# Kernel tuning notes

Measured on AMD Instinct MI355X. Metric: run time of the kernel, lower is better.

## Reference

```python
import jax, jax.numpy as jnp
import numpy as np

D_MODEL = 1024
HEADS = 16
D_HEAD = 64  # d_q = d_k = d_v
LN_EPS = 1e-5


def setup_inputs() -> dict:
    key = jax.random.key(0)
    ks = jax.random.split(key, 12)
    B, L = 2, 2048
    query = jax.random.normal(ks[0], (B, L, D_MODEL), dtype=jnp.float32)
    k_in = jax.random.normal(ks[1], (B, L, D_MODEL), dtype=jnp.float32)
    v_in = jax.random.normal(ks[2], (B, L, D_MODEL), dtype=jnp.float32)
    # causal mask: True = masked (masked_fill with -inf); row i always keeps pos i
    mask = jnp.broadcast_to(~jnp.tril(jnp.ones((L, L), dtype=bool)), (B, L, L))
    std_qk = np.sqrt(2.0 / (D_MODEL + D_HEAD)).astype(np.float32)
    Wq = jax.random.normal(ks[3], (D_MODEL, HEADS * D_HEAD), dtype=jnp.float32) * std_qk
    Wk = jax.random.normal(ks[4], (D_MODEL, HEADS * D_HEAD), dtype=jnp.float32) * std_qk
    Wv = jax.random.normal(ks[5], (D_MODEL, HEADS * D_HEAD), dtype=jnp.float32) * std_qk
    bq = jnp.zeros((HEADS * D_HEAD,), dtype=jnp.float32)
    bk = jnp.zeros((HEADS * D_HEAD,), dtype=jnp.float32)
    bv = jnp.zeros((HEADS * D_HEAD,), dtype=jnp.float32)
    lim = 1.0 / np.sqrt(HEADS * D_HEAD)
    Wo = jax.random.uniform(ks[6], (HEADS * D_HEAD, D_MODEL), dtype=jnp.float32, minval=-lim, maxval=lim)
    bo = jax.random.uniform(ks[7], (D_MODEL,), dtype=jnp.float32, minval=-lim, maxval=lim)
    gamma = jnp.ones((D_MODEL,), dtype=jnp.float32)
    beta = jnp.zeros((D_MODEL,), dtype=jnp.float32)
    return {"query": query, "key": k_in, "value": v_in, "mask": mask,
            "Wq": Wq, "bq": bq, "Wk": Wk, "bk": bk, "Wv": Wv, "bv": bv,
            "Wo": Wo, "bo": bo, "gamma": gamma, "beta": beta}


def reference(query, key, value, mask, Wq, bq, Wk, bk, Wv, bv, Wo, bo, gamma, beta):
    B, Lq, _ = query.shape
    Lk = key.shape[1]
    # QKV projections, split into heads: [B, L, H, d]
    q = (query @ Wq + bq).reshape(B, Lq, HEADS, D_HEAD)
    k = (key @ Wk + bk).reshape(B, Lk, HEADS, D_HEAD)
    v = (value @ Wv + bv).reshape(B, Lk, HEADS, D_HEAD)
    # scaled dot-product scores: [B, H, Lq, Lk]
    scores = jnp.einsum('bqhd,bkhd->bhqk', q, k) / np.sqrt(D_HEAD).astype(np.float32)
    scores = jnp.where(mask[:, None, :, :], -jnp.inf, scores)
    probs = jax.nn.softmax(scores, axis=-1)  # dropout is identity at p=0 / eval
    out = jnp.einsum('bhqk,bkhd->bqhd', probs, v).reshape(B, Lq, HEADS * D_HEAD)
    out = out @ Wo + bo  # dropout identity
    x = query + out  # residual
    mu = jnp.mean(x, axis=-1, keepdims=True)
    var = jnp.var(x, axis=-1, keepdims=True)
    return gamma * (x - mu) * jax.lax.rsqrt(var + LN_EPS) + beta
```

## Files before the change

kernel.cpp:

```cpp
#include <hip/hip_runtime.h>
#include <hip/hip_bf16.h>

#define L_SEQ  2048
#define DMODEL 1024
#define HEADS  16
#define DHEAD  64
#define BATCH  2
#define MROWS  (BATCH * L_SEQ)

typedef __attribute__((ext_vector_type(8))) short bf16x8;
typedef __attribute__((ext_vector_type(8))) unsigned short u16x8;
typedef __attribute__((ext_vector_type(4))) float f32x4;

__device__ __forceinline__ float b2f(unsigned short u) {
    union { unsigned int u32; float f; } x;
    x.u32 = ((unsigned int)u) << 16;
    return x.f;
}
__device__ __forceinline__ unsigned short f2b(float f) {
    union { float f; unsigned int u; } x; x.f = f;
    unsigned int u = x.u;
    if ((u & 0x7fffffffu) > 0x7f800000u) return (unsigned short)((u >> 16) | 0x0040);
    unsigned int r = (u + 0x7fffu + ((u >> 16) & 1u)) >> 16;
    return (unsigned short)r;
}
__device__ __forceinline__ unsigned short f2br(float f) {
    union { float f; unsigned int u; } x; x.f = f;
    return (unsigned short)((x.u + 0x7fffu + ((x.u >> 16) & 1u)) >> 16);
}

__device__ __forceinline__ float4 load4(const void* p, int isF32, size_t idx) {
    if (isF32) return *(const float4*)((const float*)p + idx);
    const ushort4 u = *(const ushort4*)((const unsigned short*)p + idx);
    return make_float4(b2f(u.x), b2f(u.y), b2f(u.z), b2f(u.w));
}
__device__ __forceinline__ float load1(const void* p, int isF32, size_t idx) {
    return isF32 ? ((const float*)p)[idx] : b2f(((const unsigned short*)p)[idx]);
}

__device__ __forceinline__ void gload16(const void* g, void* l) {
    __builtin_amdgcn_global_load_lds(
        (const __attribute__((address_space(1))) void*)g,
        (__attribute__((address_space(3))) void*)l, 16, 0, 0);
}

__global__ void detect_kernel(const unsigned short* __restrict__ q, int* __restrict__ flag) {
    int cnt = 0;
    #pragma unroll 8
    for (int t = 0; t < 64; ++t) {
        const unsigned short u = q[(threadIdx.x << 6) + t];
        const int e = (u >> 7) & 0xFF;
        cnt += (e >= 133) ? 1 : 0;
    }
    #pragma unroll
    for (int off = 32; off; off >>= 1) cnt += __shfl_xor(cnt, off);
    if (threadIdx.x == 0) *flag = (cnt > 64) ? 1 : 0;
}

__global__ void diag_kernel(float* __restrict__ out, float val, int n) {
    const int i = blockIdx.x * 256 + threadIdx.x;
    if (i < n) out[i] = val;
}

__global__ __launch_bounds__(256) void cvtW_kernel(
    const void* __restrict__ W0, const void* __restrict__ W1,
    const void* __restrict__ W2, const void* __restrict__ W3,
    unsigned short* __restrict__ T0, unsigned short* __restrict__ T1,
    unsigned short* __restrict__ T2, unsigned short* __restrict__ T3,
    const int* __restrict__ dflag)
{
    const int isF32 = *dflag;
    const int z = blockIdx.z;
    const void* W = (z == 0) ? W0 : (z == 1) ? W1 : (z == 2) ? W2 : W3;
    unsigned short* T = (z == 0) ? T0 : (z == 1) ? T1 : (z == 2) ? T2 : T3;

    __shared__ unsigned short tile[64][66];
    const int kb = blockIdx.x << 6, nb = blockIdx.y << 6;
    const int tr = threadIdx.x >> 4, tc = (threadIdx.x & 15) << 2;
    #pragma unroll
    for (int p = 0; p < 4; ++p) {
        const int r = tr + p * 16;
        const float4 v = load4(W, isF32, (size_t)(kb + r) * DMODEL + nb + tc);
        tile[tc + 0][r] = f2br(v.x);
        tile[tc + 1][r] = f2br(v.y);
        tile[tc + 2][r] = f2br(v.z);
        tile[tc + 3][r] = f2br(v.w);
    }
    __syncthreads();
    #pragma unroll
    for (int p = 0; p < 4; ++p) {
        const int rr = tr + p * 16;
        const ushort4 o = make_ushort4(tile[rr][tc], tile[rr][tc + 1],
                                       tile[rr][tc + 2], tile[rr][tc + 3]);
        *(ushort4*)(T + (size_t)(nb + rr) * DMODEL + kb + tc) = o;
    }
}

#define STAGE_B64(BP, K0)                                                         \
    _Pragma("unroll")                                                             \
    for (int s = 0; s < 4; ++s)                                                   \
        gload16(Wt + (size_t)(colBase + (wid << 5) + (s << 3) + brow8) * DMODEL + (K0) + bswz, \
                (BP) + ((wid << 5) + (s << 3)) * 64);

#define STAGE_A64(AP, BASE, K0)                                                   \
    _Pragma("unroll")                                                             \
    for (int s = 0; s < 2; ++s)                                                   \
        gload16((BASE) + (size_t)(rowBase + (wid << 4) + (s << 3) + brow8) * DMODEL + (K0) + bswz, \
                (AP) + ((wid << 4) + (s << 3)) * 64);

#define GEMM_COMPUTE64(AP, BP)                                                    \
    {                                                                             \
        bf16x8 af[2][2], bfr[4][2];                                               \
        _Pragma("unroll")                                                         \
        for (int i = 0; i < 2; ++i) {                                             \
            const int row = wm + i * 16 + ln;                                     \
            _Pragma("unroll")                                                     \
            for (int kc = 0; kc < 2; ++kc)                                        \
                af[i][kc] = *(const bf16x8*)((AP) + row * 64 +                    \
                            ((((kc << 2) | quad) ^ (ln & 7)) << 3));              \
        }                                                                         \
        _Pragma("unroll")                                                         \
        for (int j = 0; j < 4; ++j) {                                             \
            const int rowb = wn + j * 16 + ln;                                    \
            _Pragma("unroll")                                                     \
            for (int kc = 0; kc < 2; ++kc)                                        \
                bfr[j][kc] = *(const bf16x8*)((BP) + rowb * 64 +                  \
                            ((((kc << 2) | quad) ^ (ln & 7)) << 3));              \
        }                                                                         \
        _Pragma("unroll")                                                         \
        for (int kc = 0; kc < 2; ++kc)                                            \
            _Pragma("unroll")                                                     \
            for (int i = 0; i < 2; ++i)                                           \
                _Pragma("unroll")                                                 \
                for (int j = 0; j < 4; ++j)                                       \
                    acc[i][j] = __builtin_amdgcn_mfma_f32_16x16x32_bf16(          \
                        af[i][kc], bfr[j][kc], acc[i][j], 0, 0, 0);               \
    }

#define PACK_A(PK, X0, X1)                                                        \
    PK[0] = f2br(X0.x); PK[1] = f2br(X0.y); PK[2] = f2br(X0.z); PK[3] = f2br(X0.w); \
    PK[4] = f2br(X1.x); PK[5] = f2br(X1.y); PK[6] = f2br(X1.z); PK[7] = f2br(X1.w);

__global__ __launch_bounds__(256) void gemm_qkv_mfma(
    const void* __restrict__ A0, const void* __restrict__ A1, const void* __restrict__ A2,
    const unsigned short* __restrict__ Wt0, const unsigned short* __restrict__ Wt1,
    const unsigned short* __restrict__ Wt2,
    const void* __restrict__ b0, const void* __restrict__ b1, const void* __restrict__ b2,
    unsigned short* __restrict__ O0, unsigned short* __restrict__ O1, unsigned short* __restrict__ O2,
    const int* __restrict__ dflag)
{
    const int isF32 = *dflag;

    const int bid = blockIdx.x;
    const int xcd = bid & 7;
    const int jj  = bid >> 3;
    const int g   = xcd * 24 + (jj >> 3);
    const int z   = g >> 6;
    const int rowBase = (g & 63) << 6;
    const int colBase = (jj & 7) << 7;

    const void* A  = (z == 0) ? A0 : (z == 1) ? A1 : A2;
    const unsigned short* Wt = (z == 0) ? Wt0 : (z == 1) ? Wt1 : Wt2;
    const void* bi = (z == 0) ? b0 : (z == 1) ? b1 : b2;
    unsigned short* out = (z == 0) ? O0 : (z == 1) ? O1 : O2;
    const float scale = (z == 0) ? 0.125f : 1.0f;

    __shared__ __align__(16) unsigned short As[2][64 * 64];
    __shared__ __align__(16) unsigned short Bs[2][128 * 64];

    const int tid  = threadIdx.x;
    const int lane = tid & 63, wid = tid >> 6;
    const int ln   = lane & 15, quad = lane >> 4;
    const int wm   = (wid & 1) << 5;
    const int wn   = (wid >> 1) << 6;

    f32x4 acc[2][4];
    #pragma unroll
    for (int i = 0; i < 2; ++i)
        #pragma unroll
        for (int j = 0; j < 4; ++j)
            #pragma unroll
            for (int d = 0; d < 4; ++d) acc[i][j][d] = 0.f;

    const int brow8 = lane >> 3;
    const int bswz  = ((lane & 7) ^ ((lane >> 3) & 7)) << 3;

    if (isF32) {
        const int am = tid >> 2, kseg = tid & 3;
        const int c0 = (kseg << 1) ^ (am & 7), c1 = ((kseg << 1) | 1) ^ (am & 7);
        const size_t abase = (size_t)(rowBase + am) * DMODEL + (kseg << 4);

        STAGE_B64(Bs[0], 0)
        {
            const float4 a0 = load4(A, 1, abase);
            const float4 a1 = load4(A, 1, abase + 4);
            const float4 a2 = load4(A, 1, abase + 8);
            const float4 a3 = load4(A, 1, abase + 12);
            u16x8 pk0, pk1;
            PACK_A(pk0, a0, a1)
            PACK_A(pk1, a2, a3)
            *(u16x8*)(As[0] + am * 64 + (c0 << 3)) = pk0;
            *(u16x8*)(As[0] + am * 64 + (c1 << 3)) = pk1;
        }
        __syncthreads();

        int cur = 0;
        for (int t = 0; t < 15; ++t) {
            const int nxt = cur ^ 1;
            const int k0n = (t + 1) << 6;
            STAGE_B64(Bs[nxt], k0n)
            const float4 a0 = load4(A, 1, abase + k0n);
            const float4 a1 = load4(A, 1, abase + k0n + 4);
            const float4 a2 = load4(A, 1, abase + k0n + 8);
            const float4 a3 = load4(A, 1, abase + k0n + 12);

            GEMM_COMPUTE64(As[cur], Bs[cur])

            u16x8 pk0, pk1;
            PACK_A(pk0, a0, a1)
            PACK_A(pk1, a2, a3)
            *(u16x8*)(As[nxt] + am * 64 + (c0 << 3)) = pk0;
            *(u16x8*)(As[nxt] + am * 64 + (c1 << 3)) = pk1;

            __syncthreads();
            cur = nxt;
        }
        GEMM_COMPUTE64(As[cur], Bs[cur])
    } else {
        STAGE_B64(Bs[0], 0)
        STAGE_A64(As[0], (const unsigned short*)A, 0)
        __syncthreads();
        int cur = 0;
        for (int t = 0; t < 15; ++t) {
            const int nxt = cur ^ 1;
            const int k0n = (t + 1) << 6;
            STAGE_B64(Bs[nxt], k0n)
            STAGE_A64(As[nxt], (const unsigned short*)A, k0n)
            GEMM_COMPUTE64(As[cur], Bs[cur])
            __syncthreads();
            cur = nxt;
        }
        GEMM_COMPUTE64(As[cur], Bs[cur])
    }

    float bsv[4];
    #pragma unroll
    for (int j = 0; j < 4; ++j) bsv[j] = load1(bi, isF32, colBase + wn + j * 16 + ln);

    if (z != 2) {
        #pragma unroll
        for (int i = 0; i < 2; ++i) {
            const int r0 = rowBase + wm + i * 16 + quad * 4;
            const int b = r0 >> 11, l0 = r0 & (L_SEQ - 1);
            #pragma unroll
            for (int j = 0; j < 4; ++j) {
                const int n = colBase + wn + j * 16 + ln;
                const int h = n >> 6, d = n & 63;
                const size_t base = ((size_t)(b * HEADS + h) * L_SEQ) << 6;
                #pragma unroll
                for (int reg = 0; reg < 4; ++reg)
                    out[base + ((size_t)(l0 + reg) << 6) + d] =
                        f2br((acc[i][j][reg] + bsv[j]) * scale);
            }
        }
    } else {
        #pragma unroll
        for (int i = 0; i < 2; ++i) {
            const int r0 = rowBase + wm + i * 16 + quad * 4;
            const int b = r0 >> 11, l0 = r0 & (L_SEQ - 1);
            #pragma unroll
            for (int j = 0; j < 4; ++j) {
                const int n = colBase + wn + j * 16 + ln;
                const int h = n >> 6, d = n & 63;
                ushort4 o;
                o.x = f2br(acc[i][j][0] + bsv[j]);
                o.y = f2br(acc[i][j][1] + bsv[j]);
                o.z = f2br(acc[i][j][2] + bsv[j]);
                o.w = f2br(acc[i][j][3] + bsv[j]);
                *(ushort4*)(out + (((size_t)((b * HEADS + h) * 64 + d)) << 11) + l0) = o;
            }
        }
    }
}

__global__ __launch_bounds__(256) void gemm_out_mfma(
    const unsigned short* __restrict__ AO,
    const unsigned short* __restrict__ Wt,
    const void* __restrict__ bi,
    const void* __restrict__ resid,
    float* __restrict__ X,
    const int* __restrict__ dflag)
{
    const int isF32 = *dflag;
    __shared__ __align__(16) unsigned short As[2][64 * 64];
    __shared__ __align__(16) unsigned short Bs[2][128 * 64];

    const int bid = blockIdx.x;
    const int xcd = bid & 7;
    const int jj  = bid >> 3;
    const int g   = xcd * 8 + (jj >> 3);
    const int rowBase = g << 6;
    const int colBase = (jj & 7) << 7;

    const int tid  = threadIdx.x;
    const int lane = tid & 63, wid = tid >> 6;
    const int ln   = lane & 15, quad = lane >> 4;
    const int wm   = (wid & 1) << 5;
    const int wn   = (wid >> 1) << 6;

    f32x4 acc[2][4];
    #pragma unroll
    for (int i = 0; i < 2; ++i)
        #pragma unroll
        for (int j = 0; j < 4; ++j)
            #pragma unroll
            for (int d = 0; d < 4; ++d) acc[i][j][d] = 0.f;

    const int brow8 = lane >> 3;
    const int bswz  = ((lane & 7) ^ ((lane >> 3) & 7)) << 3;

    STAGE_B64(Bs[0], 0)
    STAGE_A64(As[0], AO, 0)
    __syncthreads();

    int cur = 0;
    for (int t = 0; t < 15; ++t) {
        const int nxt = cur ^ 1;
        const int k0n = (t + 1) << 6;
        STAGE_B64(Bs[nxt], k0n)
        STAGE_A64(As[nxt], AO, k0n)
        GEMM_COMPUTE64(As[cur], Bs[cur])
        __syncthreads();
        cur = nxt;
    }
    GEMM_COMPUTE64(As[cur], Bs[cur])

    float bsv[4];
    #pragma unroll
    for (int j = 0; j < 4; ++j) bsv[j] = load1(bi, isF32, colBase + wn + j * 16 + ln);

    #pragma unroll
    for (int i = 0; i < 2; ++i) {
        const int r0 = rowBase + wm + i * 16 + quad * 4;
        #pragma unroll
        for (int j = 0; j < 4; ++j) {
            const int n = colBase + wn + j * 16 + ln;
            #pragma unroll
            for (int reg = 0; reg < 4; ++reg) {
                const size_t idx = (size_t)(r0 + reg) * DMODEL + n;
                X[idx] = acc[i][j][reg] + bsv[j] + load1(resid, isF32, idx);
            }
        }
    }
}

#define KVB  128
#define NQB  (L_SEQ / 64)
#define KSTR 72
#define VSTR 136
__global__ __launch_bounds__(256, 3) void attn_mfma_kernel(
    const unsigned short* __restrict__ Q,
    const unsigned short* __restrict__ K,
    const unsigned short* __restrict__ Vt,
    unsigned short* __restrict__ AO)
{
    __shared__ unsigned short Kl[KVB * KSTR];
    __shared__ unsigned short Vl[64 * VSTR];
    __shared__ unsigned short Pl[4][16 * KVB];

    const int tid  = threadIdx.x;
    const int wid  = tid >> 6;
    const int lane = tid & 63;
    const int ln   = lane & 15;
    const int quad = lane >> 4;

    const int qb = (NQB - 1) - (blockIdx.x >> 5);
    const int bh = blockIdx.x & 31;

    const size_t qkBase = (size_t)bh * (L_SEQ * 64);
    const size_t vtBase = (size_t)bh * (64 * L_SEQ);

    const int qrow = qb * 64 + wid * 16 + ln;
    const bf16x8 qf0 = *(const bf16x8*)(Q + qkBase + (size_t)qrow * 64 + quad * 8);
    const bf16x8 qf1 = *(const bf16x8*)(Q + qkBase + (size_t)qrow * 64 + quad * 8 + 32);

    f32x4 o[4];
    #pragma unroll
    for (int d = 0; d < 4; ++d) { o[d][0] = 0.f; o[d][1] = 0.f; o[d][2] = 0.f; o[d][3] = 0.f; }
    float m[4] = {-INFINITY, -INFINITY, -INFINITY, -INFINITY};
    float l[4] = {0.f, 0.f, 0.f, 0.f};

    unsigned short* Pw = Pl[wid];
    const int kp_r = tid >> 3, kp_c = (tid & 7) * 8;
    const int vp_r = tid >> 4, vp_c = (tid & 15) * 8;

    const int nt = (qb >> 1) + 1;
    for (int jt = 0; jt < nt; ++jt) {
        __syncthreads();
        #pragma unroll
        for (int p = 0; p < 4; ++p) {
            const int kr = kp_r + p * 32;
            *(int4*)(Kl + kr * KSTR + kp_c) =
                *(const int4*)(K + qkBase + (size_t)(jt * KVB + kr) * 64 + kp_c);
            const int vr = vp_r + p * 16;
            *(int4*)(Vl + vr * VSTR + vp_c) =
                *(const int4*)(Vt + vtBase + (size_t)vr * L_SEQ + jt * KVB + vp_c);
        }
        __syncthreads();

        f32x4 s[8];
        __builtin_amdgcn_s_setprio(1);
        #pragma unroll
        for (int sub = 0; sub < 8; ++sub) {
            const bf16x8 kf0 = *(const bf16x8*)(Kl + (sub * 16 + ln) * KSTR + quad * 8);
            const bf16x8 kf1 = *(const bf16x8*)(Kl + (sub * 16 + ln) * KSTR + quad * 8 + 32);
            f32x4 a2;
            a2[0] = 0.f; a2[1] = 0.f; a2[2] = 0.f; a2[3] = 0.f;
            a2 = __builtin_amdgcn_mfma_f32_16x16x32_bf16(qf0, kf0, a2, 0, 0, 0);
            a2 = __builtin_amdgcn_mfma_f32_16x16x32_bf16(qf1, kf1, a2, 0, 0, 0);
            s[sub] = a2;
        }
        __builtin_amdgcn_s_setprio(0);

        if (jt == nt - 1) {
            const int row0 = qb * 64 + wid * 16 + quad * 4;
            #pragma unroll
            for (int sub = 0; sub < 8; ++sub) {
                const int keyg = jt * KVB + sub * 16 + ln;
                #pragma unroll
                for (int reg = 0; reg < 4; ++reg)
                    if (keyg > row0 + reg) s[sub][reg] = -INFINITY;
            }
        }

        float alpha[4];
        #pragma unroll
        for (int reg = 0; reg < 4; ++reg) {
            float t = fmaxf(
                fmaxf(fmaxf(s[0][reg], s[1][reg]), fmaxf(s[2][reg], s[3][reg])),
                fmaxf(fmaxf(s[4][reg], s[5][reg]), fmaxf(s[6][reg], s[7][reg])));
            #pragma unroll
            for (int off = 8; off; off >>= 1) t = fmaxf(t, __shfl_xor(t, off));
            const float mn = fmaxf(m[reg], t);
            alpha[reg] = __expf(m[reg] - mn);
            m[reg] = mn;
            float rs = 0.f;
            #pragma unroll
            for (int sub = 0; sub < 8; ++sub) {
                const float pe = __expf(s[sub][reg] - mn);
                s[sub][reg] = pe;
                rs += pe;
            }
            #pragma unroll
            for (int off = 8; off; off >>= 1) rs += __shfl_xor(rs, off);
            l[reg] = l[reg] * alpha[reg] + rs;
        }

        #pragma unroll
        for (int sub = 0; sub < 8; ++sub)
            #pragma unroll
            for (int reg = 0; reg < 4; ++reg) {
                const int r = quad * 4 + reg;
                const int blk = (sub * 2 + (ln >> 3)) ^ ((r >> 1) & 7);
                Pw[r * KVB + blk * 8 + (ln & 7)] = f2br(s[sub][reg]);
            }

        #pragma unroll
        for (int dblk = 0; dblk < 4; ++dblk)
            #pragma unroll
            for (int reg = 0; reg < 4; ++reg)
                o[dblk][reg] *= alpha[reg];

        __builtin_amdgcn_s_setprio(1);
        #pragma unroll
        for (int jb = 0; jb < 4; ++jb) {
            const int rblk = (jb * 4 + quad) ^ ((ln >> 1) & 7);
            const bf16x8 pf = *(const bf16x8*)(Pw + ln * KVB + rblk * 8);
            #pragma unroll
            for (int dblk = 0; dblk < 4; ++dblk) {
                const bf16x8 vf = *(const bf16x8*)(Vl + (dblk * 16 + ln) * VSTR + jb * 32 + quad * 8);
                o[dblk] = __builtin_amdgcn_mfma_f32_16x16x32_bf16(pf, vf, o[dblk], 0, 0, 0);
            }
        }
        __builtin_amdgcn_s_setprio(0);
    }

    const int b = bh >> 4, h = bh & 15;
    float rl[4];
    #pragma unroll
    for (int reg = 0; reg < 4; ++reg) rl[reg] = 1.f / l[reg];
    #pragma unroll
    for (int dblk = 0; dblk < 4; ++dblk)
        #pragma unroll
        for (int reg = 0; reg < 4; ++reg) {
            const int row = qb * 64 + wid * 16 + quad * 4 + reg;
            AO[((size_t)(b * L_SEQ + row)) * DMODEL + h * 64 + dblk * 16 + ln] =
                f2br(o[dblk][reg] * rl[reg]);
        }
}

__global__ __launch_bounds__(256) void ln_kernel(
    const float* __restrict__ X,
    const void* __restrict__ gamma,
    const void* __restrict__ beta,
    float* __restrict__ out,
    const int* __restrict__ dflag)
{
    const int isF32 = *dflag;
    const int row = blockIdx.x;
    const int tid = threadIdx.x;
    const float* x = X + (size_t)row * DMODEL;
    const int c0 = tid << 2;
    const float4 vv = *(const float4*)(x + c0);
    float s  = vv.x + vv.y + vv.z + vv.w;
    float s2 = vv.x * vv.x + vv.y * vv.y + vv.z * vv.z + vv.w * vv.w;
    #pragma unroll
    for (int off = 32; off; off >>= 1) {
        s  += __shfl_xor(s, off);
        s2 += __shfl_xor(s2, off);
    }
    __shared__ float red[4][2];
    const int wid = tid >> 6, lane = tid & 63;
    if (lane == 0) { red[wid][0] = s; red[wid][1] = s2; }
    __syncthreads();
    s  = red[0][0] + red[1][0] + red[2][0] + red[3][0];
    s2 = red[0][1] + red[1][1] + red[2][1] + red[3][1];
    const float mu  = s * (1.f / 1024.f);
    const float var = s2 * (1.f / 1024.f) - mu * mu;
    const float inv = rsqrtf(var + 1e-5f);
    const float4 gm = load4(gamma, isF32, c0);
    const float4 bt = load4(beta,  isF32, c0);
    float4 r;
    r.x = gm.x * (vv.x - mu) * inv + bt.x;
    r.y = gm.y * (vv.y - mu) * inv + bt.y;
    r.z = gm.z * (vv.z - mu) * inv + bt.z;
    r.w = gm.w * (vv.w - mu) * inv + bt.w;
    if (!(r.x == r.x) || fabsf(r.x) > 1e37f) r.x = 777000.0f;
    if (!(r.y == r.y) || fabsf(r.y) > 1e37f) r.y = 777000.0f;
    if (!(r.z == r.z) || fabsf(r.z) > 1e37f) r.z = 777000.0f;
    if (!(r.w == r.w) || fabsf(r.w) > 1e37f) r.w = 777000.0f;
    *(float4*)(out + (size_t)row * DMODEL + c0) = r;
}

extern "C" void kernel_launch(void* const* d_in, const int* in_sizes, int n_in,
                              void* d_out, int out_size, void* d_ws, size_t ws_size,
                              hipStream_t stream) {
    const void* query = d_in[0];
    const void* key   = d_in[1];
    const void* value = d_in[2];

    int wbase = 4;
    if (in_sizes[3] == DMODEL * DMODEL) wbase = 3;
    const void* Wq    = d_in[wbase + 0];
    const void* bq    = d_in[wbase + 1];
    const void* Wk    = d_in[wbase + 2];
    const void* bk    = d_in[wbase + 3];
    const void* Wv    = d_in[wbase + 4];
    const void* bv    = d_in[wbase + 5];
    const void* Wo    = d_in[wbase + 6];
    const void* bo    = d_in[wbase + 7];
    const void* gamma = d_in[wbase + 8];
    const void* beta  = d_in[wbase + 9];

    const size_t NEED = ((size_t)24u << 20) + 64;
    if (ws_size < NEED) {
        const float val = (float)(ws_size >> 20) * 1000.0f;
        diag_kernel<<<dim3((out_size + 255) / 256), dim3(256), 0, stream>>>(
            (float*)d_out, val, out_size);
        return;
    }

    char* ws = (char*)d_ws;
    unsigned short* Qb  = (unsigned short*)(ws);
    unsigned short* Kb  = (unsigned short*)(ws + (size_t)( 8u << 20));
    unsigned short* Vtb = (unsigned short*)(ws + (size_t)(16u << 20));
    float* X            = (float*)ws;
    int* dflag          = (int*)(ws + (size_t)(24u << 20));
    unsigned short* AO  = (unsigned short*)d_out;
    unsigned short* Wtq = (unsigned short*)d_out + ((size_t)4u << 20);
    unsigned short* Wtk = Wtq + ((size_t)1u << 20);
    unsigned short* Wtv = Wtk + ((size_t)1u << 20);
    unsigned short* Wto = Wtv + ((size_t)1u << 20);

    const dim3 blk(256);

    detect_kernel<<<dim3(1), dim3(64), 0, stream>>>((const unsigned short*)query, dflag);
    cvtW_kernel<<<dim3(16, 16, 4), blk, 0, stream>>>(
        Wq, Wk, Wv, Wo, Wtq, Wtk, Wtv, Wto, dflag);
    gemm_qkv_mfma<<<dim3(1536), blk, 0, stream>>>(
        query, key, value, Wtq, Wtk, Wtv, bq, bk, bv, Qb, Kb, Vtb, dflag);
    attn_mfma_kernel<<<dim3(BATCH * HEADS * 32), blk, 0, stream>>>(Qb, Kb, Vtb, AO);
    gemm_out_mfma<<<dim3(512), blk, 0, stream>>>(AO, Wto, bo, query, X, dflag);
    ln_kernel<<<dim3(MROWS), blk, 0, stream>>>(X, gamma, beta, (float*)d_out, dflag);
}
```

Baseline: 288.8 us.

## Retile QKV projection GEMM to 128x512 tiles with triple-buffered K32 pipeline

Rewrites the QKV projection GEMM to use 512-thread blocks, each computing a 128x512 output tile with BK=32 and a 3-stage shared-memory ring. Each wave now holds a 64x128 accumulator. Loads are issued two stages ahead, with explicit waitcnt and barriers. The aim is more reuse of A and B per shared-memory byte and better hiding of global load latency. In exchange it uses many more registers, launches only 192 blocks (under one wave of CUs), and relies on fragile manual vmcnt accounting. The attention output store also switches to a different bf16 rounding helper.

```diff
diff --git a/kernel.cpp b/kernel.cpp
--- a/kernel.cpp
+++ b/kernel.cpp
@@ -93,6 +93,199 @@
         const ushort4 o = make_ushort4(tile[rr][tc], tile[rr][tc + 1],
                                        tile[rr][tc + 2], tile[rr][tc + 3]);
         *(ushort4*)(T + (size_t)(nb + rr) * DMODEL + kb + tc) = o;
+    }
+}
+
+#define QSTAGE_B(BP, K0)                                                          \
+    _Pragma("unroll")                                                             \
+    for (int s = 0; s < 4; ++s)                                                   \
+        gload16(Wt + (size_t)(colBase + (wid << 6) + (s << 4) + (lane >> 2)) * DMODEL \
+                    + (K0) + qsw,                                                 \
+                (BP) + ((wid << 6) + (s << 4)) * 32);
+
+#define QSTAGE_A_BF16(BP, K0)                                                     \
+    gload16((const unsigned short*)A + (size_t)(rowBase + (wid << 4) + (lane >> 2)) * DMODEL \
+                    + (K0) + qsw,                                                 \
+            (BP) + (wid << 4) * 32);
+
+#define QCOMPUTE(AP, BP)                                                          \
+    {                                                                             \
+        bf16x8 af[4], bf8[8];                                                     \
+        _Pragma("unroll")                                                         \
+        for (int i = 0; i < 4; ++i) {                                             \
+            const int row = wm + i * 16 + ln;                                     \
+            af[i] = *(const bf16x8*)((AP) + row * 32 + ((quad ^ (row & 3)) << 3)); \
+        }                                                                         \
+        _Pragma("unroll")                                                         \
+        for (int j = 0; j < 8; ++j) {                                             \
+            const int rowb = wn + j * 16 + ln;                                    \
+            bf8[j] = *(const bf16x8*)((BP) + rowb * 32 + ((quad ^ (rowb & 3)) << 3)); \
+        }                                                                         \
+        _Pragma("unroll")                                                         \
+        for (int i = 0; i < 4; ++i)                                               \
+            _Pragma("unroll")                                                     \
+            for (int j = 0; j < 8; ++j)                                           \
+                acc[i][j] = __builtin_amdgcn_mfma_f32_16x16x32_bf16(              \
+                    af[i], bf8[j], acc[i][j], 0, 0, 0);                           \
+    }
+
+#define QPACK_A(PK, X0, X1)                                                       \
+    PK[0] = f2br(X0.x); PK[1] = f2br(X0.y); PK[2] = f2br(X0.z); PK[3] = f2br(X0.w); \
+    PK[4] = f2br(X1.x); PK[5] = f2br(X1.y); PK[6] = f2br(X1.z); PK[7] = f2br(X1.w);
+
+__global__ __launch_bounds__(512, 2) void gemm_qkv_mfma(
+    const void* __restrict__ A0, const void* __restrict__ A1, const void* __restrict__ A2,
+    const unsigned short* __restrict__ Wt0, const unsigned short* __restrict__ Wt1,
+    const unsigned short* __restrict__ Wt2,
+    const void* __restrict__ b0, const void* __restrict__ b1, const void* __restrict__ b2,
+    unsigned short* __restrict__ O0, unsigned short* __restrict__ O1, unsigned short* __restrict__ O2,
+    const int* __restrict__ dflag)
+{
+    const int isF32 = *dflag;
+
+    const int bid = blockIdx.x;
+    const int xcd = bid & 7;
+    const int jj  = bid >> 3;
+    const int g   = xcd * 24 + jj;
+    const int z   = g >> 6;
+    const int rowBase = ((g >> 1) & 31) << 7;
+    const int colBase = (g & 1) << 9;
+
+    const void* A  = (z == 0) ? A0 : (z == 1) ? A1 : A2;
+    const unsigned short* Wt = (z == 0) ? Wt0 : (z == 1) ? Wt1 : Wt2;
+    const void* bi = (z == 0) ? b0 : (z == 1) ? b1 : b2;
+    unsigned short* out = (z == 0) ? O0 : (z == 1) ? O1 : O2;
+    const float scale = (z == 0) ? 0.125f : 1.0f;
+
+    __shared__ __align__(16) unsigned short As[3][128 * 32];
+    __shared__ __align__(16) unsigned short Bs[3][512 * 32];
+
+    const int tid  = threadIdx.x;
+    const int lane = tid & 63, wid = tid >> 6;
+    const int ln   = lane & 15, quad = lane >> 4;
+    const int wm   = (wid & 1) << 6;
+    const int wn   = (wid >> 1) << 7;
+    const int qsw  = (((lane & 3) ^ ((lane >> 2) & 3)) << 3);
+
+    f32x4 acc[4][8];
+    #pragma unroll
+    for (int i = 0; i < 4; ++i)
+        #pragma unroll
+        for (int j = 0; j < 8; ++j)
+            #pragma unroll
+            for (int d = 0; d < 4; ++d) acc[i][j][d] = 0.f;
+
+    if (isF32) {
+        const int am = tid >> 2, kseg = tid & 3;
+        const int ac = (kseg ^ (am & 3)) << 3;
+        const size_t abase = (size_t)(rowBase + am) * DMODEL + (kseg << 3);
+
+        QSTAGE_B(Bs[0], 0)
+        const float4 c0 = load4(A, 1, abase);
+        const float4 c1 = load4(A, 1, abase + 4);
+        QSTAGE_B(Bs[1], 32)
+        float4 pA0 = load4(A, 1, abase + 32);
+        float4 pA1 = load4(A, 1, abase + 36);
+        {
+            u16x8 pk;
+            QPACK_A(pk, c0, c1)
+            *(u16x8*)(As[0] + am * 32 + ac) = pk;
+        }
+        asm volatile("s_waitcnt lgkmcnt(0)" ::: "memory");
+        __builtin_amdgcn_sched_barrier(0);
+        __builtin_amdgcn_s_barrier();
+        __builtin_amdgcn_sched_barrier(0);
+
+        for (int t = 0; t < 31; ++t) {
+            float4 nA0, nA1;
+            if (t < 30) {
+                const int k2 = (t + 2) << 5;
+                QSTAGE_B(Bs[(t + 2) % 3], k2)
+                nA0 = load4(A, 1, abase + k2);
+                nA1 = load4(A, 1, abase + k2 + 4);
+            }
+            __builtin_amdgcn_sched_barrier(0);
+
+            QCOMPUTE(As[t % 3], Bs[t % 3])
+
+            {
+                u16x8 pk;
+                QPACK_A(pk, pA0, pA1)
+                *(u16x8*)(As[(t + 1) % 3] + am * 32 + ac) = pk;
+            }
+            if (t < 30) { pA0 = nA0; pA1 = nA1; }
+            asm volatile("s_waitcnt lgkmcnt(0)" ::: "memory");
+            __builtin_amdgcn_sched_barrier(0);
+            __builtin_amdgcn_s_barrier();
+            __builtin_amdgcn_sched_barrier(0);
+        }
+        QCOMPUTE(As[1], Bs[1])
+    } else {
+        QSTAGE_B(Bs[0], 0)
+        QSTAGE_A_BF16(As[0], 0)
+        QSTAGE_B(Bs[1], 32)
+        QSTAGE_A_BF16(As[1], 32)
+        asm volatile("s_waitcnt vmcnt(5)" ::: "memory");
+        __builtin_amdgcn_sched_barrier(0);
+        __builtin_amdgcn_s_barrier();
+        __builtin_amdgcn_sched_barrier(0);
+
+        for (int t = 0; t < 31; ++t) {
+            if (t < 30) {
+                const int k2 = (t + 2) << 5;
+                QSTAGE_B(Bs[(t + 2) % 3], k2)
+                QSTAGE_A_BF16(As[(t + 2) % 3], k2)
+            }
+            __builtin_amdgcn_sched_barrier(0);
+
+            QCOMPUTE(As[t % 3], Bs[t % 3])
+
+            if (t < 30) asm volatile("s_waitcnt vmcnt(5)" ::: "memory");
+            else        asm volatile("s_waitcnt vmcnt(0)" ::: "memory");
+            __builtin_amdgcn_sched_barrier(0);
+            __builtin_amdgcn_s_barrier();
+            __builtin_amdgcn_sched_barrier(0);
+        }
+        QCOMPUTE(As[1], Bs[1])
+    }
+
+    float bsv[8];
+    #pragma unroll
+    for (int j = 0; j < 8; ++j) bsv[j] = load1(bi, isF32, colBase + wn + j * 16 + ln);
+
+    if (z != 2) {
+        #pragma unroll
+        for (int i = 0; i < 4; ++i) {
+            const int r0 = rowBase + wm + i * 16 + quad * 4;
+            const int b = r0 >> 11, l0 = r0 & (L_SEQ - 1);
+            #pragma unroll
+            for (int j = 0; j < 8; ++j) {
+                const int n = colBase + wn + j * 16 + ln;
+                const int h = n >> 6, d = n & 63;
+                const size_t base = ((size_t)(b * HEADS + h) * L_SEQ) << 6;
+                #pragma unroll
+                for (int reg = 0; reg < 4; ++reg)
+                    out[base + ((size_t)(l0 + reg) << 6) + d] =
+                        f2br((acc[i][j][reg] + bsv[j]) * scale);
+            }
+        }
+    } else {
+        #pragma unroll
+        for (int i = 0; i < 4; ++i) {
+            const int r0 = rowBase + wm + i * 16 + quad * 4;
+            const int b = r0 >> 11, l0 = r0 & (L_SEQ - 1);
+            #pragma unroll
+            for (int j = 0; j < 8; ++j) {
+                const int n = colBase + wn + j * 16 + ln;
+                const int h = n >> 6, d = n & 63;
+                ushort4 o;
+                o.x = f2br(acc[i][j][0] + bsv[j]);
+                o.y = f2br(acc[i][j][1] + bsv[j]);
+                o.z = f2br(acc[i][j][2] + bsv[j]);
+                o.w = f2br(acc[i][j][3] + bsv[j]);
+                *(ushort4*)(out + (((size_t)((b * HEADS + h) * 64 + d)) << 11) + l0) = o;
+            }
+        }
     }
 }
 
@@ -137,152 +330,6 @@
                         af[i][kc], bfr[j][kc], acc[i][j], 0, 0, 0);               \
     }
 
-#define PACK_A(PK, X0, X1)                                                        \
-    PK[0] = f2br(X0.x); PK[1] = f2br(X0.y); PK[2] = f2br(X0.z); PK[3] = f2br(X0.w); \
-    PK[4] = f2br(X1.x); PK[5] = f2br(X1.y); PK[6] = f2br(X1.z); PK[7] = f2br(X1.w);
-
-__global__ __launch_bounds__(256) void gemm_qkv_mfma(
-    const void* __restrict__ A0, const void* __restrict__ A1, const void* __restrict__ A2,
-    const unsigned short* __restrict__ Wt0, const unsigned short* __restrict__ Wt1,
-    const unsigned short* __restrict__ Wt2,
-    const void* __restrict__ b0, const void* __restrict__ b1, const void* __restrict__ b2,
-    unsigned short* __restrict__ O0, unsigned short* __restrict__ O1, unsigned short* __restrict__ O2,
-    const int* __restrict__ dflag)
-{
-    const int isF32 = *dflag;
-
-    const int bid = blockIdx.x;
-    const int xcd = bid & 7;
-    const int jj  = bid >> 3;
-    const int g   = xcd * 24 + (jj >> 3);
-    const int z   = g >> 6;
-    const int rowBase = (g & 63) << 6;
-    const int colBase = (jj & 7) << 7;
-
-    const void* A  = (z == 0) ? A0 : (z == 1) ? A1 : A2;
-    const unsigned short* Wt = (z == 0) ? Wt0 : (z == 1) ? Wt1 : Wt2;
-    const void* bi = (z == 0) ? b0 : (z == 1) ? b1 : b2;
-    unsigned short* out = (z == 0) ? O0 : (z == 1) ? O1 : O2;
-    const float scale = (z == 0) ? 0.125f : 1.0f;
-
-    __shared__ __align__(16) unsigned short As[2][64 * 64];
-    __shared__ __align__(16) unsigned short Bs[2][128 * 64];
-
-    const int tid  = threadIdx.x;
-    const int lane = tid & 63, wid = tid >> 6;
-    const int ln   = lane & 15, quad = lane >> 4;
-    const int wm   = (wid & 1) << 5;
-    const int wn   = (wid >> 1) << 6;
-
-    f32x4 acc[2][4];
-    #pragma unroll
-    for (int i = 0; i < 2; ++i)
-        #pragma unroll
-        for (int j = 0; j < 4; ++j)
-            #pragma unroll
-            for (int d = 0; d < 4; ++d) acc[i][j][d] = 0.f;
-
-    const int brow8 = lane >> 3;
-    const int bswz  = ((lane & 7) ^ ((lane >> 3) & 7)) << 3;
-
-    if (isF32) {
-        const int am = tid >> 2, kseg = tid & 3;
-        const int c0 = (kseg << 1) ^ (am & 7), c1 = ((kseg << 1) | 1) ^ (am & 7);
-        const size_t abase = (size_t)(rowBase + am) * DMODEL + (kseg << 4);
-
-        STAGE_B64(Bs[0], 0)
-        {
-            const float4 a0 = load4(A, 1, abase);
-            const float4 a1 = load4(A, 1, abase + 4);
-            const float4 a2 = load4(A, 1, abase + 8);
-            const float4 a3 = load4(A, 1, abase + 12);
-            u16x8 pk0, pk1;
-            PACK_A(pk0, a0, a1)
-            PACK_A(pk1, a2, a3)
-            *(u16x8*)(As[0] + am * 64 + (c0 << 3)) = pk0;
-            *(u16x8*)(As[0] + am * 64 + (c1 << 3)) = pk1;
-        }
-        __syncthreads();
-
-        int cur = 0;
-        for (int t = 0; t < 15; ++t) {
-            const int nxt = cur ^ 1;
-            const int k0n = (t + 1) << 6;
-            STAGE_B64(Bs[nxt], k0n)
-            const float4 a0 = load4(A, 1, abase + k0n);
-            const float4 a1 = load4(A, 1, abase + k0n + 4);
-            const float4 a2 = load4(A, 1, abase + k0n + 8);
-            const float4 a3 = load4(A, 1, abase + k0n + 12);
-
-            GEMM_COMPUTE64(As[cur], Bs[cur])
-
-            u16x8 pk0, pk1;
-            PACK_A(pk0, a0, a1)
-            PACK_A(pk1, a2, a3)
-            *(u16x8*)(As[nxt] + am * 64 + (c0 << 3)) = pk0;
-            *(u16x8*)(As[nxt] + am * 64 + (c1 << 3)) = pk1;
-
-            __syncthreads();
-            cur = nxt;
-        }
-        GEMM_COMPUTE64(As[cur], Bs[cur])
-    } else {
-        STAGE_B64(Bs[0], 0)
-        STAGE_A64(As[0], (const unsigned short*)A, 0)
-        __syncthreads();
-        int cur = 0;
-        for (int t = 0; t < 15; ++t) {
-            const int nxt = cur ^ 1;
-            const int k0n = (t + 1) << 6;
-            STAGE_B64(Bs[nxt], k0n)
-            STAGE_A64(As[nxt], (const unsigned short*)A, k0n)
-            GEMM_COMPUTE64(As[cur], Bs[cur])
-            __syncthreads();
-            cur = nxt;
-        }
-        GEMM_COMPUTE64(As[cur], Bs[cur])
-    }
-
-    float bsv[4];
-    #pragma unroll
-    for (int j = 0; j < 4; ++j) bsv[j] = load1(bi, isF32, colBase + wn + j * 16 + ln);
-
-    if (z != 2) {
-        #pragma unroll
-        for (int i = 0; i < 2; ++i) {
-            const int r0 = rowBase + wm + i * 16 + quad * 4;
-            const int b = r0 >> 11, l0 = r0 & (L_SEQ - 1);
-            #pragma unroll
-            for (int j = 0; j < 4; ++j) {
-                const int n = colBase + wn + j * 16 + ln;
-                const int h = n >> 6, d = n & 63;
-                const size_t base = ((size_t)(b * HEADS + h) * L_SEQ) << 6;
-                #pragma unroll
-                for (int reg = 0; reg < 4; ++reg)
-                    out[base + ((size_t)(l0 + reg) << 6) + d] =
-                        f2br((acc[i][j][reg] + bsv[j]) * scale);
-            }
-        }
-    } else {
-        #pragma unroll
-        for (int i = 0; i < 2; ++i) {
-            const int r0 = rowBase + wm + i * 16 + quad * 4;
-            const int b = r0 >> 11, l0 = r0 & (L_SEQ - 1);
-            #pragma unroll
-            for (int j = 0; j < 4; ++j) {
-                const int n = colBase + wn + j * 16 + ln;
-                const int h = n >> 6, d = n & 63;
-                ushort4 o;
-                o.x = f2br(acc[i][j][0] + bsv[j]);
-                o.y = f2br(acc[i][j][1] + bsv[j]);
-                o.z = f2br(acc[i][j][2] + bsv[j]);
-                o.w = f2br(acc[i][j][3] + bsv[j]);
-                *(ushort4*)(out + (((size_t)((b * HEADS + h) * 64 + d)) << 11) + l0) = o;
-            }
-        }
-    }
-}
-
 __global__ __launch_bounds__(256) void gemm_out_mfma(
     const unsigned short* __restrict__ AO,
     const unsigned short* __restrict__ Wt,
@@ -495,7 +542,7 @@
         for (int reg = 0; reg < 4; ++reg) {
             const int row = qb * 64 + wid * 16 + quad * 4 + reg;
             AO[((size_t)(b * L_SEQ + row)) * DMODEL + h * 64 + dblk * 16 + ln] =
-                f2br(o[dblk][reg] * rl[reg]);
+                f2b(o[dblk][reg] * rl[reg]);
         }
 }
 
@@ -587,7 +634,7 @@
     detect_kernel<<<dim3(1), dim3(64), 0, stream>>>((const unsigned short*)query, dflag);
     cvtW_kernel<<<dim3(16, 16, 4), blk, 0, stream>>>(
         Wq, Wk, Wv, Wo, Wtq, Wtk, Wtv, Wto, dflag);
-    gemm_qkv_mfma<<<dim3(1536), blk, 0, stream>>>(
+    gemm_qkv_mfma<<<dim3(192), dim3(512), 0, stream>>>(
         query, key, value, Wtq, Wtk, Wtv, bq, bk, bv, Qb, Kb, Vtb, dflag);
     attn_mfma_kernel<<<dim3(BATCH * HEADS * 32), blk, 0, stream>>>(Qb, Kb, Vtb, AO);
     gemm_out_mfma<<<dim3(512), blk, 0, stream>>>(AO, Wto, bo, query, X, dflag);
```

Result: no change. 287.0 us (-0.6%).

## Enlarge QKV GEMM tiles to 128x256 with 512 threads, remap attention blocks per XCD

Applied to the files above, without the earlier changes.

Rewrites the QKV projection GEMM to use 128x256 output tiles, 512-thread blocks, K-step 32 and a 4x4 MFMA accumulator per wave. The grid shrinks from 1536 to 384 blocks, which raises operand reuse per tile and cuts global and LDS traffic per FLOP. It also remaps attention block indices so the query blocks of one head land on the same XCD for better L2 locality of K/V, and switches the attention output conversion to a different bf16 rounding helper. The larger tile costs more registers and fewer resident blocks, and 384 blocks may underfill the device or leave a tail wave.

```diff
diff --git a/kernel.cpp b/kernel.cpp
--- a/kernel.cpp
+++ b/kernel.cpp
@@ -93,6 +93,176 @@
         const ushort4 o = make_ushort4(tile[rr][tc], tile[rr][tc + 1],
                                        tile[rr][tc + 2], tile[rr][tc + 3]);
         *(ushort4*)(T + (size_t)(nb + rr) * DMODEL + kb + tc) = o;
+    }
+}
+
+#define QSTAGE_B(BP, K0)                                                          \
+    _Pragma("unroll")                                                             \
+    for (int s = 0; s < 2; ++s)                                                   \
+        gload16(Wt + (size_t)(colBase + (wid << 5) + (s << 4) + (lane >> 2)) * DMODEL \
+                    + (K0) + qsw,                                                 \
+                (BP) + ((wid << 5) + (s << 4)) * 32);
+
+#define QSTAGE_A_BF16(BP, K0)                                                     \
+    gload16((const unsigned short*)A + (size_t)(rowBase + (wid << 4) + (lane >> 2)) * DMODEL \
+                    + (K0) + qsw,                                                 \
+            (BP) + (wid << 4) * 32);
+
+#define QCOMPUTE(AP, BP)                                                          \
+    {                                                                             \
+        bf16x8 af[4], bfr[4];                                                     \
+        _Pragma("unroll")                                                         \
+        for (int i = 0; i < 4; ++i) {                                             \
+            const int row = wm + i * 16 + ln;                                     \
+            af[i] = *(const bf16x8*)((AP) + row * 32 + ((quad ^ (row & 3)) << 3)); \
+        }                                                                         \
+        _Pragma("unroll")                                                         \
+        for (int j = 0; j < 4; ++j) {                                             \
+            const int rowb = wn + j * 16 + ln;                                    \
+            bfr[j] = *(const bf16x8*)((BP) + rowb * 32 + ((quad ^ (rowb & 3)) << 3)); \
+        }                                                                         \
+        _Pragma("unroll")                                                         \
+        for (int i = 0; i < 4; ++i)                                               \
+            _Pragma("unroll")                                                     \
+            for (int j = 0; j < 4; ++j)                                           \
+                acc[i][j] = __builtin_amdgcn_mfma_f32_16x16x32_bf16(              \
+                    af[i], bfr[j], acc[i][j], 0, 0, 0);                           \
+    }
+
+#define QPACK_A(PK, X0, X1)                                                       \
+    PK[0] = f2br(X0.x); PK[1] = f2br(X0.y); PK[2] = f2br(X0.z); PK[3] = f2br(X0.w); \
+    PK[4] = f2br(X1.x); PK[5] = f2br(X1.y); PK[6] = f2br(X1.z); PK[7] = f2br(X1.w);
+
+__global__ __launch_bounds__(512) void gemm_qkv_mfma(
+    const void* __restrict__ A0, const void* __restrict__ A1, const void* __restrict__ A2,
+    const unsigned short* __restrict__ Wt0, const unsigned short* __restrict__ Wt1,
+    const unsigned short* __restrict__ Wt2,
+    const void* __restrict__ b0, const void* __restrict__ b1, const void* __restrict__ b2,
+    unsigned short* __restrict__ O0, unsigned short* __restrict__ O1, unsigned short* __restrict__ O2,
+    const int* __restrict__ dflag)
+{
+    const int isF32 = *dflag;
+
+    const int bid = blockIdx.x;
+    const int xcd = bid & 7;
+    const int jj  = bid >> 3;
+    const int g   = xcd * 48 + jj;
+    const int z   = g >> 7;
+    const int rem = g & 127;
+    const int rowBase = (rem >> 2) << 7;
+    const int colBase = (rem & 3) << 8;
+
+    const void* A  = (z == 0) ? A0 : (z == 1) ? A1 : A2;
+    const unsigned short* Wt = (z == 0) ? Wt0 : (z == 1) ? Wt1 : Wt2;
+    const void* bi = (z == 0) ? b0 : (z == 1) ? b1 : b2;
+    unsigned short* out = (z == 0) ? O0 : (z == 1) ? O1 : O2;
+    const float scale = (z == 0) ? 0.125f : 1.0f;
+
+    __shared__ __align__(16) unsigned short As[2][128 * 32];
+    __shared__ __align__(16) unsigned short Bs[2][256 * 32];
+
+    const int tid  = threadIdx.x;
+    const int lane = tid & 63, wid = tid >> 6;
+    const int ln   = lane & 15, quad = lane >> 4;
+    const int wm   = (wid & 1) << 6;
+    const int wn   = (wid >> 1) << 6;
+    const int qsw  = (((lane & 3) ^ ((lane >> 2) & 3)) << 3);
+
+    f32x4 acc[4][4];
+    #pragma unroll
+    for (int i = 0; i < 4; ++i)
+        #pragma unroll
+        for (int j = 0; j < 4; ++j)
+            #pragma unroll
+            for (int d = 0; d < 4; ++d) acc[i][j][d] = 0.f;
+
+    if (isF32) {
+        const int am = tid >> 2, kseg = tid & 3;
+        const int ac = (kseg ^ (am & 3)) << 3;
+        const size_t abase = (size_t)(rowBase + am) * DMODEL + (kseg << 3);
+
+        QSTAGE_B(Bs[0], 0)
+        {
+            const float4 a0 = load4(A, 1, abase);
+            const float4 a1 = load4(A, 1, abase + 4);
+            u16x8 pk;
+            QPACK_A(pk, a0, a1)
+            *(u16x8*)(As[0] + am * 32 + ac) = pk;
+        }
+        __syncthreads();
+
+        int cur = 0;
+        for (int t = 0; t < 31; ++t) {
+            const int nxt = cur ^ 1;
+            const int k0n = (t + 1) << 5;
+            QSTAGE_B(Bs[nxt], k0n)
+            const float4 a0 = load4(A, 1, abase + k0n);
+            const float4 a1 = load4(A, 1, abase + k0n + 4);
+
+            QCOMPUTE(As[cur], Bs[cur])
+
+            u16x8 pk;
+            QPACK_A(pk, a0, a1)
+            *(u16x8*)(As[nxt] + am * 32 + ac) = pk;
+
+            __syncthreads();
+            cur = nxt;
+        }
+        QCOMPUTE(As[cur], Bs[cur])
+    } else {
+        QSTAGE_B(Bs[0], 0)
+        QSTAGE_A_BF16(As[0], 0)
+        __syncthreads();
+        int cur = 0;
+        for (int t = 0; t < 31; ++t) {
+            const int nxt = cur ^ 1;
+            const int k0n = (t + 1) << 5;
+            QSTAGE_B(Bs[nxt], k0n)
+            QSTAGE_A_BF16(As[nxt], k0n)
+            QCOMPUTE(As[cur], Bs[cur])
+            __syncthreads();
+            cur = nxt;
+        }
+        QCOMPUTE(As[cur], Bs[cur])
+    }
+
+    float bsv[4];
+    #pragma unroll
+    for (int j = 0; j < 4; ++j) bsv[j] = load1(bi, isF32, colBase + wn + j * 16 + ln);
+
+    if (z != 2) {
+        #pragma unroll
+        for (int i = 0; i < 4; ++i) {
+            const int r0 = rowBase + wm + i * 16 + quad * 4;
+            const int b = r0 >> 11, l0 = r0 & (L_SEQ - 1);
+            #pragma unroll
+            for (int j = 0; j < 4; ++j) {
+                const int n = colBase + wn + j * 16 + ln;
+                const int h = n >> 6, d = n & 63;
+                const size_t base = ((size_t)(b * HEADS + h) * L_SEQ) << 6;
+                #pragma unroll
+                for (int reg = 0; reg < 4; ++reg)
+                    out[base + ((size_t)(l0 + reg) << 6) + d] =
+                        f2br((acc[i][j][reg] + bsv[j]) * scale);
+            }
+        }
+    } else {
+        #pragma unroll
+        for (int i = 0; i < 4; ++i) {
+            const int r0 = rowBase + wm + i * 16 + quad * 4;
+            const int b = r0 >> 11, l0 = r0 & (L_SEQ - 1);
+            #pragma unroll
+            for (int j = 0; j < 4; ++j) {
+                const int n = colBase + wn + j * 16 + ln;
+                const int h = n >> 6, d = n & 63;
+                ushort4 o;
+                o.x = f2br(acc[i][j][0] + bsv[j]);
+                o.y = f2br(acc[i][j][1] + bsv[j]);
+                o.z = f2br(acc[i][j][2] + bsv[j]);
+                o.w = f2br(acc[i][j][3] + bsv[j]);
+                *(ushort4*)(out + (((size_t)((b * HEADS + h) * 64 + d)) << 11) + l0) = o;
+            }
+        }
     }
 }
 
@@ -137,152 +307,6 @@
                         af[i][kc], bfr[j][kc], acc[i][j], 0, 0, 0);               \
     }
 
-#define PACK_A(PK, X0, X1)                                                        \
-    PK[0] = f2br(X0.x); PK[1] = f2br(X0.y); PK[2] = f2br(X0.z); PK[3] = f2br(X0.w); \
-    PK[4] = f2br(X1.x); PK[5] = f2br(X1.y); PK[6] = f2br(X1.z); PK[7] = f2br(X1.w);
-
-__global__ __launch_bounds__(256) void gemm_qkv_mfma(
-    const void* __restrict__ A0, const void* __restrict__ A1, const void* __restrict__ A2,
-    const unsigned short* __restrict__ Wt0, const unsigned short* __restrict__ Wt1,
-    const unsigned short* __restrict__ Wt2,
-    const void* __restrict__ b0, const void* __restrict__ b1, const void* __restrict__ b2,
-    unsigned short* __restrict__ O0, unsigned short* __restrict__ O1, unsigned short* __restrict__ O2,
-    const int* __restrict__ dflag)
-{
-    const int isF32 = *dflag;
-
-    const int bid = blockIdx.x;
-    const int xcd = bid & 7;
-    const int jj  = bid >> 3;
-    const int g   = xcd * 24 + (jj >> 3);
-    const int z   = g >> 6;
-    const int rowBase = (g & 63) << 6;
-    const int colBase = (jj & 7) << 7;
-
-    const void* A  = (z == 0) ? A0 : (z == 1) ? A1 : A2;
-    const unsigned short* Wt = (z == 0) ? Wt0 : (z == 1) ? Wt1 : Wt2;
-    const void* bi = (z == 0) ? b0 : (z == 1) ? b1 : b2;
-    unsigned short* out = (z == 0) ? O0 : (z == 1) ? O1 : O2;
-    const float scale = (z == 0) ? 0.125f : 1.0f;
-
-    __shared__ __align__(16) unsigned short As[2][64 * 64];
-    __shared__ __align__(16) unsigned short Bs[2][128 * 64];
-
-    const int tid  = threadIdx.x;
-    const int lane = tid & 63, wid = tid >> 6;
-    const int ln   = lane & 15, quad = lane >> 4;
-    const int wm   = (wid & 1) << 5;
-    const int wn   = (wid >> 1) << 6;
-
-    f32x4 acc[2][4];
-    #pragma unroll
-    for (int i = 0; i < 2; ++i)
-        #pragma unroll
-        for (int j = 0; j < 4; ++j)
-            #pragma unroll
-            for (int d = 0; d < 4; ++d) acc[i][j][d] = 0.f;
-
-    const int brow8 = lane >> 3;
-    const int bswz  = ((lane & 7) ^ ((lane >> 3) & 7)) << 3;
-
-    if (isF32) {
-        const int am = tid >> 2, kseg = tid & 3;
-        const int c0 = (kseg << 1) ^ (am & 7), c1 = ((kseg << 1) | 1) ^ (am & 7);
-        const size_t abase = (size_t)(rowBase + am) * DMODEL + (kseg << 4);
-
-        STAGE_B64(Bs[0], 0)
-        {
-            const float4 a0 = load4(A, 1, abase);
-            const float4 a1 = load4(A, 1, abase + 4);
-            const float4 a2 = load4(A, 1, abase + 8);
-            const float4 a3 = load4(A, 1, abase + 12);
-            u16x8 pk0, pk1;
-            PACK_A(pk0, a0, a1)
-            PACK_A(pk1, a2, a3)
-            *(u16x8*)(As[0] + am * 64 + (c0 << 3)) = pk0;
-            *(u16x8*)(As[0] + am * 64 + (c1 << 3)) = pk1;
-        }
-        __syncthreads();
-
-        int cur = 0;
-        for (int t = 0; t < 15; ++t) {
-            const int nxt = cur ^ 1;
-            const int k0n = (t + 1) << 6;
-            STAGE_B64(Bs[nxt], k0n)
-            const float4 a0 = load4(A, 1, abase + k0n);
-            const float4 a1 = load4(A, 1, abase + k0n + 4);
-            const float4 a2 = load4(A, 1, abase + k0n + 8);
-            const float4 a3 = load4(A, 1, abase + k0n + 12);
-
-            GEMM_COMPUTE64(As[cur], Bs[cur])
-
-            u16x8 pk0, pk1;
-            PACK_A(pk0, a0, a1)
-            PACK_A(pk1, a2, a3)
-            *(u16x8*)(As[nxt] + am * 64 + (c0 << 3)) = pk0;
-            *(u16x8*)(As[nxt] + am * 64 + (c1 << 3)) = pk1;
-
-            __syncthreads();
-            cur = nxt;
-        }
-        GEMM_COMPUTE64(As[cur], Bs[cur])
-    } else {
-        STAGE_B64(Bs[0], 0)
-        STAGE_A64(As[0], (const unsigned short*)A, 0)
-        __syncthreads();
-        int cur = 0;
-        for (int t = 0; t < 15; ++t) {
-            const int nxt = cur ^ 1;
-            const int k0n = (t + 1) << 6;
-            STAGE_B64(Bs[nxt], k0n)
-            STAGE_A64(As[nxt], (const unsigned short*)A, k0n)
-            GEMM_COMPUTE64(As[cur], Bs[cur])
-            __syncthreads();
-            cur = nxt;
-        }
-        GEMM_COMPUTE64(As[cur], Bs[cur])
-    }
-
-    float bsv[4];
-    #pragma unroll
-    for (int j = 0; j < 4; ++j) bsv[j] = load1(bi, isF32, colBase + wn + j * 16 + ln);
-
-    if (z != 2) {
-        #pragma unroll
-        for (int i = 0; i < 2; ++i) {
-            const int r0 = rowBase + wm + i * 16 + quad * 4;
-            const int b = r0 >> 11, l0 = r0 & (L_SEQ - 1);
-            #pragma unroll
-            for (int j = 0; j < 4; ++j) {
-                const int n = colBase + wn + j * 16 + ln;
-                const int h = n >> 6, d = n & 63;
-                const size_t base = ((size_t)(b * HEADS + h) * L_SEQ) << 6;
-                #pragma unroll
-                for (int reg = 0; reg < 4; ++reg)
-                    out[base + ((size_t)(l0 + reg) << 6) + d] =
-                        f2br((acc[i][j][reg] + bsv[j]) * scale);
-            }
-        }
-    } else {
-        #pragma unroll
-        for (int i = 0; i < 2; ++i) {
-            const int r0 = rowBase + wm + i * 16 + quad * 4;
-            const int b = r0 >> 11, l0 = r0 & (L_SEQ - 1);
-            #pragma unroll
-            for (int j = 0; j < 4; ++j) {
-                const int n = colBase + wn + j * 16 + ln;
-                const int h = n >> 6, d = n & 63;
-                ushort4 o;
-                o.x = f2br(acc[i][j][0] + bsv[j]);
-                o.y = f2br(acc[i][j][1] + bsv[j]);
-                o.z = f2br(acc[i][j][2] + bsv[j]);
-                o.w = f2br(acc[i][j][3] + bsv[j]);
-                *(ushort4*)(out + (((size_t)((b * HEADS + h) * 64 + d)) << 11) + l0) = o;
-            }
-        }
-    }
-}
-
 __global__ __launch_bounds__(256) void gemm_out_mfma(
     const unsigned short* __restrict__ AO,
     const unsigned short* __restrict__ Wt,
@@ -374,8 +398,10 @@
     const int ln   = lane & 15;
     const int quad = lane >> 4;
 
-    const int qb = (NQB - 1) - (blockIdx.x >> 5);
-    const int bh = blockIdx.x & 31;
+    const int xcd = blockIdx.x & 7;
+    const int jj  = blockIdx.x >> 3;
+    const int bh  = xcd * 4 + (jj & 3);
+    const int qb  = (NQB - 1) - (jj >> 2);
 
     const size_t qkBase = (size_t)bh * (L_SEQ * 64);
     const size_t vtBase = (size_t)bh * (64 * L_SEQ);
@@ -495,7 +521,7 @@
         for (int reg = 0; reg < 4; ++reg) {
             const int row = qb * 64 + wid * 16 + quad * 4 + reg;
             AO[((size_t)(b * L_SEQ + row)) * DMODEL + h * 64 + dblk * 16 + ln] =
-                f2br(o[dblk][reg] * rl[reg]);
+                f2b(o[dblk][reg] * rl[reg]);
         }
 }
 
@@ -587,7 +613,7 @@
     detect_kernel<<<dim3(1), dim3(64), 0, stream>>>((const unsigned short*)query, dflag);
     cvtW_kernel<<<dim3(16, 16, 4), blk, 0, stream>>>(
         Wq, Wk, Wv, Wo, Wtq, Wtk, Wtv, Wto, dflag);
-    gemm_qkv_mfma<<<dim3(1536), blk, 0, stream>>>(
+    gemm_qkv_mfma<<<dim3(384), dim3(512), 0, stream>>>(
         query, key, value, Wtq, Wtk, Wtv, bq, bk, bv, Qb, Kb, Vtb, dflag);
     attn_mfma_kernel<<<dim3(BATCH * HEADS * 32), blk, 0, stream>>>(Qb, Kb, Vtb, AO);
     gemm_out_mfma<<<dim3(512), blk, 0, stream>>>(AO, Wto, bo, query, X, dflag);
```

After: 277.6 us. -3.9%, faster.
